# Kernel optimization log

Hardware: AMD Instinct MI355X
Metric: run time of the kernel (lower is better)

The kernel has to match this reference:

```python
import jax, jax.numpy as jnp
import numpy as np

EPS = 1e-6
ROPE_THETA = 10000.0


def rmsnorm(x, w):
    return x * jax.lax.rsqrt(jnp.mean(x * x, axis=-1, keepdims=True) + EPS) * w


def rope(q, k, seq_len, head_dim):
    # rotate-half RoPE. q,k: [b, h, s, d]
    half = head_dim // 2
    inv_freq = 1.0 / (ROPE_THETA ** (jnp.arange(0, half, dtype=jnp.float32) / half))
    t = jnp.arange(seq_len, dtype=jnp.float32)
    freqs = jnp.outer(t, inv_freq)                      # [s, d/2]
    cos = jnp.concatenate([jnp.cos(freqs)] * 2, axis=-1)  # [s, d]
    sin = jnp.concatenate([jnp.sin(freqs)] * 2, axis=-1)

    def rot(x):
        x1, x2 = x[..., :half], x[..., half:]
        return jnp.concatenate([-x2, x1], axis=-1)

    return q * cos + rot(q) * sin, k * cos + rot(k) * sin


def setup_inputs() -> dict:
    key = jax.random.key(0)
    ks = jax.random.split(key, 8)
    B, S, D, E, F = 4, 2048, 1024, 8, 4096
    sd = 0.02
    return {
        "x": jax.random.normal(ks[0], (B, S, D), dtype=jnp.float32),
        "mapped_tokens": jax.random.randint(ks[1], (B, S), 0, E, dtype=jnp.int32),
        "rms1_w": jnp.ones((D,), dtype=jnp.float32),
        "wqkv": jax.random.normal(ks[2], (D, 3 * D), dtype=jnp.float32) * sd,
        "wo": jax.random.normal(ks[3], (D, D), dtype=jnp.float32) * sd,
        "rms2_w": jnp.ones((D,), dtype=jnp.float32),
        "w1": jax.random.normal(ks[4], (E, D, F), dtype=jnp.float32) * sd,
        "w2": jax.random.normal(ks[5], (E, F, D), dtype=jnp.float32) * sd,
    }


def attention(x, wqkv, wo, num_heads=16):
    B, S, D = x.shape
    hd = D // num_heads
    qkv = x @ wqkv                                       # [b, s, 3D]
    q, k, v = jnp.split(qkv, 3, axis=-1)
    def heads(t):
        return t.reshape(B, S, num_heads, hd).transpose(0, 2, 1, 3)  # [b,h,s,d]
    q, k, v = heads(q), heads(k), heads(v)
    q, k = rope(q, k, S, hd)
    scores = jnp.einsum("bhqd,bhkd->bhqk", q, k) / jnp.sqrt(jnp.float32(hd))
    causal = jnp.tril(jnp.ones((S, S), dtype=bool))
    scores = jnp.where(causal, scores, jnp.finfo(scores.dtype).min)
    attn = jax.nn.softmax(scores, axis=-1)
    out = jnp.einsum("bhqk,bhkd->bhqd", attn, v)
    out = out.transpose(0, 2, 1, 3).reshape(B, S, D)
    return out @ wo


def moe_hash_ffn(x, mapped_tokens, w1, w2):
    # hash-routed MoE: each token goes to exactly one expert given by mapped_tokens
    B, S, D = x.shape
    E = w1.shape[0]
    xf = x.reshape(B * S, D)
    mt = mapped_tokens.reshape(B * S)
    out = jnp.zeros_like(xf)
    for e in range(E):  # small fixed expert count
        y = jax.nn.gelu(xf @ w1[e]) @ w2[e]
        out = out + jnp.where((mt == e)[:, None], y, 0.0)
    return out.reshape(B, S, D)


def reference(x, mapped_tokens, rms1_w, wqkv, wo, rms2_w, w1, w2):
    h = x + attention(rmsnorm(x, rms1_w), wqkv, wo)
    out = h + moe_hash_ffn(rmsnorm(h, rms2_w), mapped_tokens, w1, w2)
    return out
```

## Files before the change

kernel.cpp:

```cpp
#include <hip/hip_runtime.h>
#include <hip/hip_bf16.h>
#include <stdint.h>

typedef __hip_bfloat16 bf16;
typedef __attribute__((ext_vector_type(8))) short bf16x8;
typedef __attribute__((ext_vector_type(4))) float f32x4;
typedef __attribute__((ext_vector_type(16))) float f32x16;
typedef unsigned int u32;

static constexpr int Bsz = 4, S = 2048, D = 1024, E = 8, F = 4096, NH = 16, HD = 64;
static constexpr int TOK = Bsz * S;
static constexpr int SLOTS = TOK + E * 128;

#define DEV __device__ __forceinline__

DEV void async16(const bf16* g, bf16* l) {
  __builtin_amdgcn_global_load_lds((const __attribute__((address_space(1))) u32*)g,
                                   (__attribute__((address_space(3))) u32*)l, 16, 0, 0);
}

DEV u32 lds_off(const bf16* p) {
  return (u32)(uintptr_t)(__attribute__((address_space(3))) bf16*)p;
}

DEV bf16x8 dsr128(u32 addr) {
  bf16x8 d;
  asm volatile("ds_read_b128 %0, %1" : "=v"(d) : "v"(addr));
  return d;
}

DEV float gelu_fast(float x) {
  const float z = 0.7978845608028654f * (x + 0.044715f * x * x * x);
  return x / (1.f + __expf(-2.f * z));
}

DEV u32 cvtpk(float lo, float hi) {
  u32 r;
  asm("v_cvt_pk_bf16_f32 %0, %1, %2" : "=v"(r) : "v"(lo), "v"(hi));
  return r;
}


__global__ void cvt_transpose(const float* __restrict__ in, bf16* __restrict__ out, int R, int C) {
  __shared__ float t[64][65];
  const size_t zoff = (size_t)blockIdx.z * R * C;
  const int c0 = blockIdx.x * 64, r0 = blockIdx.y * 64;
  const int tid = threadIdx.x;
  const int lrow = tid >> 4, lcol = (tid & 15) * 4;
#pragma unroll
  for (int p = 0; p < 4; ++p) {
    const int r = lrow + p * 16;
    const float4 v = *(const float4*)(in + zoff + (size_t)(r0 + r) * C + c0 + lcol);
    t[r][lcol] = v.x; t[r][lcol + 1] = v.y; t[r][lcol + 2] = v.z; t[r][lcol + 3] = v.w;
  }
  __syncthreads();
  const int ow = tid >> 3, je = (tid & 7) * 8;
#pragma unroll
  for (int p = 0; p < 2; ++p) {
    const int oc = ow + p * 32;
    union { bf16x8 v; bf16 b[8]; } o8;
#pragma unroll
    for (int j = 0; j < 8; ++j) o8.b[j] = __float2bfloat16(t[je + j][oc]);
    *(bf16x8*)(out + zoff + (size_t)(c0 + oc) * R + r0 + je) = o8.v;
  }
}

__global__ void rope_tables(float* __restrict__ cosT, float* __restrict__ sinT) {
  const int s = blockIdx.x * 2 + (threadIdx.x >> 5);
  const int i = threadIdx.x & 31;
  const float inv_freq = powf(10000.f, -(float)i / 32.f);
  const float ang = (float)s * inv_freq;
  cosT[s * 32 + i] = cosf(ang);
  sinT[s * 32 + i] = sinf(ang);
}

__global__ void rmsnorm_k(const float* __restrict__ x, const float* __restrict__ w, bf16* __restrict__ out) {
  const size_t row = blockIdx.x;
  const int tid = threadIdx.x;
  const float4 v = *(const float4*)(x + row * D + tid * 4);
  float ss = v.x * v.x + v.y * v.y + v.z * v.z + v.w * v.w;
#pragma unroll
  for (int off = 1; off < 64; off <<= 1) ss += __shfl_xor(ss, off);
  __shared__ float red[4];
  if ((tid & 63) == 0) red[tid >> 6] = ss;
  __syncthreads();
  const float inv = rsqrtf((red[0] + red[1] + red[2] + red[3]) * (1.f / D) + 1e-6f);
  const float4 wv = *(const float4*)(w + tid * 4);
  union { ushort4 u; bf16 b[4]; } o;
  o.b[0] = __float2bfloat16(v.x * inv * wv.x);
  o.b[1] = __float2bfloat16(v.y * inv * wv.y);
  o.b[2] = __float2bfloat16(v.z * inv * wv.z);
  o.b[3] = __float2bfloat16(v.w * inv * wv.w);
  *(ushort4*)((unsigned short*)out + row * D + tid * 4) = o.u;
}

__global__ void route_init(int* counts, int* cursors, int* perm) {
  const int i = blockIdx.x * 256 + threadIdx.x;
  if (i < E) { counts[i] = 0; cursors[i] = 0; }
  if (i < SLOTS) perm[i] = -1;
}
__global__ void route_count(const int* __restrict__ mt, int* counts) {
  const int i = blockIdx.x * 256 + threadIdx.x;
  if (i < TOK) atomicAdd(&counts[mt[i]], 1);
}
__global__ void route_offsets(const int* __restrict__ counts, int* aoff) {
  if (threadIdx.x == 0) {
    int off = 0; aoff[0] = 0;
    for (int e = 0; e < E; ++e) { off += (counts[e] + 127) & ~127; aoff[e + 1] = off; }
  }
}
__global__ void route_scatter(const int* __restrict__ mt, const int* __restrict__ aoff,
                              int* cursors, int* perm) {
  const int i = blockIdx.x * 256 + threadIdx.x;
  if (i < TOK) { const int e = mt[i]; perm[aoff[e] + atomicAdd(&cursors[e], 1)] = i; }
}

__global__ __launch_bounds__(512) void qkv8p(
    const bf16* __restrict__ A, const bf16* __restrict__ Bt,
    const float* __restrict__ c_t, const float* __restrict__ s_t,
    bf16* __restrict__ o_q, bf16* __restrict__ o_k, bf16* __restrict__ o_v) {
  constexpr int K = 1024, NT = K / 64;
  __shared__ __align__(16) bf16 LA[2][256 * 64];
  __shared__ __align__(16) bf16 LB[2][256 * 64];
  const int tid = threadIdx.x;
  const int lane = tid & 63, wv = tid >> 6;
  const int wm = wv >> 2, wn = wv & 3;
  const int rl = lane & 15, kg = lane >> 4;
  const int gx = gridDim.x;
  const int nwg = gx * gridDim.y;
  int bid = blockIdx.y * gx + blockIdx.x;
  bid = (bid & 7) * (nwg >> 3) + (bid >> 3);
  const int nbase = (bid % gx) * 256, mbase = (bid / gx) * 256;
  f32x4 acc[8][4] = {};
  const int srow = tid >> 3;
  const int sc = (tid & 7) ^ ((srow >> 1) & 7);
  const bf16* Ag = A + (size_t)(mbase + srow) * K + sc * 8;
  const bf16* Bg = Bt + (size_t)(nbase + srow) * K + sc * 8;

  auto stage = [&](int t, int h) {
    const int buf = t & 1;
    const int mat = h >> 1, rh = h & 1;
    const bf16* src = (mat ? Bg : Ag) + (size_t)(rh * 128) * K + t * 64;
    bf16* dst = (mat ? &LB[buf][0] : &LA[buf][0]) + rh * 128 * 64 + tid * 8;
    async16(src, dst);
    async16(src + (size_t)64 * K, dst + 64 * 64);
  };

  bf16x8 bfr[4];
  auto phaseC = [&](int t, int ks, int mih, bool loadB) {
    const int buf = t & 1;
    const u32 ab = lds_off(&LA[buf][0]);
    const u32 bb = lds_off(&LB[buf][0]);
    bf16x8 af[4];
#pragma unroll
    for (int mi = 0; mi < 4; ++mi) {
      const int row = wm * 128 + mih * 64 + mi * 16 + rl;
      const u32 ph = (u32)((ks * 4 + kg) ^ ((row >> 1) & 7));
      af[mi] = dsr128(ab + (u32)row * 128 + ph * 16);
    }
    if (loadB) {
#pragma unroll
      for (int ni = 0; ni < 4; ++ni) {
        const int row = wn * 64 + ni * 16 + rl;
        const u32 ph = (u32)((ks * 4 + kg) ^ ((row >> 1) & 7));
        bfr[ni] = dsr128(bb + (u32)row * 128 + ph * 16);
      }
    }
    asm volatile("s_waitcnt lgkmcnt(0)" ::: "memory");
    __builtin_amdgcn_sched_barrier(0);
    __builtin_amdgcn_s_setprio(1);
#pragma unroll
    for (int mi = 0; mi < 4; ++mi)
#pragma unroll
      for (int ni = 0; ni < 4; ++ni)
        acc[mih * 4 + mi][ni] =
            __builtin_amdgcn_mfma_f32_16x16x32_bf16(af[mi], bfr[ni], acc[mih * 4 + mi][ni], 0, 0, 0);
    __builtin_amdgcn_s_setprio(0);
  };

  stage(0, 0); stage(0, 1); stage(0, 2); stage(0, 3);
  for (int t = 0; t < NT; ++t) {
    const bool more = (t + 1 < NT);
#pragma unroll
    for (int p = 0; p < 4; ++p) {
      if (p == 0) {
        if (more) {
          stage(t + 1, 0);
          asm volatile("s_waitcnt vmcnt(2)" ::: "memory");
        } else {
          asm volatile("s_waitcnt vmcnt(0)" ::: "memory");
        }
        __builtin_amdgcn_s_barrier();
        __builtin_amdgcn_sched_barrier(0);
      } else if (more) {
        stage(t + 1, p);
      }
      phaseC(t, p >> 1, p & 1, (p & 1) == 0);
      __builtin_amdgcn_s_barrier();
      __builtin_amdgcn_sched_barrier(0);
    }
  }

  const int colbase = nbase + wn * 64;
  const int part = colbase >> 10;
  const int head = (colbase & 1023) >> 6;
  const float qs = (part == 0) ? 0.18033688011112042f : 1.f;
#pragma unroll
  for (int ai = 0; ai < 8; ++ai) {
    const int rowoff = (ai >> 2) * 64 + (ai & 3) * 16;
#pragma unroll
    for (int r = 0; r < 4; ++r) {
      const int grow = mbase + wm * 128 + rowoff + kg * 4 + r;
      const int bb = grow >> 11, sp = grow & (S - 1);
      if (part == 2) {
#pragma unroll
        for (int ni = 0; ni < 4; ++ni) {
          const int d = ni * 16 + rl;
          o_v[((size_t)(bb * NH + head) * HD + d) * S + sp] = __float2bfloat16(acc[ai][ni][r]);
        }
      } else {
        bf16* dst = (part == 0) ? o_q : o_k;
        const size_t base = ((size_t)(bb * NH + head) * S + sp) * HD;
#pragma unroll
        for (int np = 0; np < 2; ++np) {
          const int i = np * 16 + rl;
          const float c = c_t[sp * 32 + i];
          const float sn = s_t[sp * 32 + i];
          const float lo = acc[ai][np][r];
          const float hi = acc[ai][np + 2][r];
          dst[base + i] = __float2bfloat16((lo * c - hi * sn) * qs);
          dst[base + i + 32] = __float2bfloat16((hi * c + lo * sn) * qs);
        }
      }
    }
  }
}

template <int EPI, int BM>
__global__ __launch_bounds__(2 * BM) void gemm_bt(
    const bf16* __restrict__ A, const bf16* __restrict__ Bt, int M, int N, int K,
    const int* __restrict__ aoff, long long estride,
    const float* __restrict__ xres, float* __restrict__ o_h,
    bf16* __restrict__ o_act,
    const int* __restrict__ perm, const float* __restrict__ hres, float* __restrict__ o_out) {
  constexpr int WN = BM / 64;
  constexpr int MR = BM / 2;
  constexpr int M_FR = MR / 16;
  __shared__ __align__(16) bf16 As[2][BM * 32];
  __shared__ __align__(16) bf16 Bs[2][BM * 32];
  const int tid = threadIdx.x;
  const int lane = tid & 63, wv = tid >> 6;
  const int wm = wv / WN, wn = wv % WN;
  const int rl = lane & 15, kg = lane >> 4;
  const int gx = gridDim.x;
  const int nwg = gx * gridDim.y;
  int bid = blockIdx.y * gx + blockIdx.x;
  bid = (bid & 7) * (nwg >> 3) + (bid >> 3);
  const int nbase = (bid % gx) * BM, mbase = (bid / gx) * BM;
  const bf16* Btp = Bt;
  if constexpr (EPI >= 2) {
    int e = 0;
#pragma unroll
    for (int t = 0; t < E - 1; ++t) e += (mbase >= aoff[t + 1]) ? 1 : 0;
    Btp = Bt + (size_t)e * estride;
  }
  f32x4 acc[M_FR][4] = {};
  const int srow = tid >> 2;
  const int sc = (tid & 3) ^ ((srow >> 1) & 3);
  const bf16* Agp[2];
#pragma unroll
  for (int c = 0; c < 2; ++c) {
    int rowslot = mbase + c * MR + srow;
    if constexpr (EPI == 2) {
      const int t = perm[rowslot];
      rowslot = (t < 0) ? 0 : t;
    }
    Agp[c] = A + (size_t)rowslot * K + sc * 8;
  }
  const bf16* Bg = Btp + (size_t)(nbase + srow) * K + sc * 8;

  auto stage = [&](int bi, int ko) {
#pragma unroll
    for (int c = 0; c < 2; ++c) {
      async16(Agp[c] + ko, &As[bi][c * MR * 32 + wv * 512]);
      async16(Bg + (size_t)(c * MR) * K + ko, &Bs[bi][c * MR * 32 + wv * 512]);
    }
  };
  auto compute = [&](int bi) {
    bf16x8 af[M_FR], bfr[4];
#pragma unroll
    for (int mi = 0; mi < M_FR; ++mi) {
      const int row = wm * MR + mi * 16 + rl;
      af[mi] = *(const bf16x8*)&As[bi][row * 32 + ((kg ^ ((row >> 1) & 3))) * 8];
    }
#pragma unroll
    for (int ni = 0; ni < 4; ++ni) {
      const int row = wn * 64 + ni * 16 + rl;
      bfr[ni] = *(const bf16x8*)&Bs[bi][row * 32 + ((kg ^ ((row >> 1) & 3))) * 8];
    }
#pragma unroll
    for (int mi = 0; mi < M_FR; ++mi)
#pragma unroll
      for (int ni = 0; ni < 4; ++ni)
        acc[mi][ni] = __builtin_amdgcn_mfma_f32_16x16x32_bf16(af[mi], bfr[ni], acc[mi][ni], 0, 0, 0);
  };

  const int nk = K >> 5;
  stage(0, 0);
  __syncthreads();
  for (int kb = 0; kb < nk; ++kb) {
    if (kb + 1 < nk) stage((kb + 1) & 1, (kb + 1) * 32);
    compute(kb & 1);
    __syncthreads();
  }

#pragma unroll
  for (int mi = 0; mi < M_FR; ++mi) {
#pragma unroll
    for (int ni = 0; ni < 4; ++ni) {
#pragma unroll
      for (int r = 0; r < 4; ++r) {
        const int grow = mbase + wm * MR + mi * 16 + kg * 4 + r;
        const int gcol = nbase + wn * 64 + ni * 16 + rl;
        const float vv = acc[mi][ni][r];
        if constexpr (EPI == 1) {
          const size_t ix = (size_t)grow * 1024 + gcol;
          o_h[ix] = xres[ix] + vv;
        } else if constexpr (EPI == 2) {
          o_act[(size_t)grow * 4096 + gcol] = __float2bfloat16(gelu_fast(vv));
        } else {
          const int t = perm[grow];
          if (t >= 0) {
            const size_t ix = (size_t)t * 1024 + gcol;
            o_out[ix] = hres[ix] + vv;
          }
        }
      }
    }
  }
}

__global__ __launch_bounds__(256, 3) void attn_kernel(const bf16* __restrict__ Qb,
                                                      const bf16* __restrict__ Kb,
                                                      const bf16* __restrict__ Vt,
                                                      bf16* __restrict__ AO) {
  __shared__ __align__(16) bf16 Kl[2][64 * 64];
  __shared__ __align__(16) bf16 Vl[2][64 * 64];
  const int bh = blockIdx.x;
  const int tid = threadIdx.x;
  const int w = tid >> 6, lane = tid & 63;
  const int q = lane & 31, hi = lane >> 5;
  const bf16* Qp = Qb + (size_t)bh * S * HD;
  const bf16* Kp = Kb + (size_t)bh * S * HD;
  const bf16* Vp = Vt + (size_t)bh * S * HD;
  const int b = bh >> 4, h = bh & 15;
  const int qblk = (S / 128 - 1) - blockIdx.y;
  const int qrow0 = qblk * 128 + w * 32;
  const int ntb = qblk * 2 + 2;
  const int ntw = (qrow0 >> 6) + 1;
  const int srow = tid >> 3;
  const int schk = tid & 7;

  bf16x8 qf[4];
#pragma unroll
  for (int t = 0; t < 4; ++t)
    qf[t] = *(const bf16x8*)(Qp + (size_t)(qrow0 + q) * HD + t * 16 + hi * 8);
  f32x16 oa0 = {}, oa1 = {};
  float m = -INFINITY, l = 0.f;

  auto stageKV = [&](int buf, int kvb) {
#pragma unroll
    for (int hh = 0; hh < 2; ++hh) {
      const int row = srow + hh * 32;
      const int c = schk ^ (row & 7);
      async16(Kp + (size_t)(kvb + row) * HD + c * 8, &Kl[buf][tid * 8 + hh * 2048]);
      async16(Vp + (size_t)row * S + kvb + c * 8, &Vl[buf][tid * 8 + hh * 2048]);
    }
  };
  auto packP = [&](float s0, float s1, float s2, float s3,
                   float s4, float s5, float s6, float s7) -> bf16x8 {
    u32 x0 = cvtpk(s0, s1), x1 = cvtpk(s2, s3);
    u32 y0 = cvtpk(s4, s5), y1 = cvtpk(s6, s7);
    asm volatile("v_permlane32_swap_b32 %0, %1" : "+v"(x0), "+v"(y0));
    asm volatile("v_permlane32_swap_b32 %0, %1" : "+v"(x1), "+v"(y1));
    union { u32 w[4]; bf16x8 v; } u;
    u.w[0] = x0; u.w[1] = x1; u.w[2] = y0; u.w[3] = y1;
    return u.v;
  };

  stageKV(0, 0);
  __syncthreads();
  for (int kt = 0; kt < ntb; ++kt) {
    const int buf = kt & 1;
    const int kvb = kt * 64;
    if (kt + 1 < ntb) stageKV(buf ^ 1, kvb + 64);
    if (kt < ntw) {
      f32x16 sa0 = {}, sa1 = {};
#pragma unroll
      for (int t = 0; t < 4; ++t) {
        const int c = (2 * t + hi) ^ (q & 7);
        const bf16x8 kf0 = *(const bf16x8*)&Kl[buf][q * 64 + c * 8];
        sa0 = __builtin_amdgcn_mfma_f32_32x32x16_bf16(kf0, qf[t], sa0, 0, 0, 0);
      }
#pragma unroll
      for (int t = 0; t < 4; ++t) {
        const int c = (2 * t + hi) ^ (q & 7);
        const bf16x8 kf1 = *(const bf16x8*)&Kl[buf][(q + 32) * 64 + c * 8];
        sa1 = __builtin_amdgcn_mfma_f32_32x32x16_bf16(kf1, qf[t], sa1, 0, 0, 0);
      }
      if (kvb + 63 > qrow0) {
#pragma unroll
        for (int r = 0; r < 16; ++r) {
          const int kloc = (r & 3) + 8 * (r >> 2) + 4 * hi;
          sa0[r] = (kvb + kloc > qrow0 + q) ? -3.0e38f : sa0[r];
          sa1[r] = (kvb + 32 + kloc > qrow0 + q) ? -3.0e38f : sa1[r];
        }
      }
      float vm;
      {
        float a0 = fmaxf(fmaxf(sa0[0], sa0[1]), fmaxf(sa0[2], sa0[3]));
        float a1 = fmaxf(fmaxf(sa0[4], sa0[5]), fmaxf(sa0[6], sa0[7]));
        float a2 = fmaxf(fmaxf(sa0[8], sa0[9]), fmaxf(sa0[10], sa0[11]));
        float a3 = fmaxf(fmaxf(sa0[12], sa0[13]), fmaxf(sa0[14], sa0[15]));
        float b0 = fmaxf(fmaxf(sa1[0], sa1[1]), fmaxf(sa1[2], sa1[3]));
        float b1 = fmaxf(fmaxf(sa1[4], sa1[5]), fmaxf(sa1[6], sa1[7]));
        float b2 = fmaxf(fmaxf(sa1[8], sa1[9]), fmaxf(sa1[10], sa1[11]));
        float b3 = fmaxf(fmaxf(sa1[12], sa1[13]), fmaxf(sa1[14], sa1[15]));
        vm = fmaxf(fmaxf(fmaxf(a0, a1), fmaxf(a2, a3)), fmaxf(fmaxf(b0, b1), fmaxf(b2, b3)));
      }
      vm = fmaxf(vm, __shfl_xor(vm, 32));
      const bool grow = __any(vm > m);
      const float mn = grow ? fmaxf(m, vm) : m;
#pragma unroll
      for (int r = 0; r < 16; ++r) {
        sa0[r] = exp2f(sa0[r] - mn);
        sa1[r] = exp2f(sa1[r] - mn);
      }
      float ps;
      {
        float a0 = (sa0[0] + sa0[1]) + (sa0[2] + sa0[3]);
        float a1 = (sa0[4] + sa0[5]) + (sa0[6] + sa0[7]);
        float a2 = (sa0[8] + sa0[9]) + (sa0[10] + sa0[11]);
        float a3 = (sa0[12] + sa0[13]) + (sa0[14] + sa0[15]);
        float b0 = (sa1[0] + sa1[1]) + (sa1[2] + sa1[3]);
        float b1 = (sa1[4] + sa1[5]) + (sa1[6] + sa1[7]);
        float b2 = (sa1[8] + sa1[9]) + (sa1[10] + sa1[11]);
        float b3 = (sa1[12] + sa1[13]) + (sa1[14] + sa1[15]);
        ps = ((a0 + a1) + (a2 + a3)) + ((b0 + b1) + (b2 + b3));
      }
      ps += __shfl_xor(ps, 32);
      if (grow) {
        const float scs = exp2f(m - mn);
        l = l * scs + ps;
        m = mn;
#pragma unroll
        for (int r = 0; r < 16; ++r) { oa0[r] *= scs; oa1[r] *= scs; }
      } else {
        l += ps;
      }
      {
        auto vrd = [&](int r, int s2i) -> bf16x8 {
          const int c = (2 * s2i + hi) ^ (r & 7);
          return *(const bf16x8*)&Vl[buf][r * 64 + c * 8];
        };
        const bf16x8 pf0 = packP(sa0[0], sa0[1], sa0[2], sa0[3], sa0[4], sa0[5], sa0[6], sa0[7]);
        oa0 = __builtin_amdgcn_mfma_f32_32x32x16_bf16(vrd(q, 0), pf0, oa0, 0, 0, 0);
        oa1 = __builtin_amdgcn_mfma_f32_32x32x16_bf16(vrd(q + 32, 0), pf0, oa1, 0, 0, 0);
        const bf16x8 pf1 = packP(sa0[8], sa0[9], sa0[10], sa0[11], sa0[12], sa0[13], sa0[14], sa0[15]);
        oa0 = __builtin_amdgcn_mfma_f32_32x32x16_bf16(vrd(q, 1), pf1, oa0, 0, 0, 0);
        oa1 = __builtin_amdgcn_mfma_f32_32x32x16_bf16(vrd(q + 32, 1), pf1, oa1, 0, 0, 0);
        const bf16x8 pf2 = packP(sa1[0], sa1[1], sa1[2], sa1[3], sa1[4], sa1[5], sa1[6], sa1[7]);
        oa0 = __builtin_amdgcn_mfma_f32_32x32x16_bf16(vrd(q, 2), pf2, oa0, 0, 0, 0);
        oa1 = __builtin_amdgcn_mfma_f32_32x32x16_bf16(vrd(q + 32, 2), pf2, oa1, 0, 0, 0);
        const bf16x8 pf3 = packP(sa1[8], sa1[9], sa1[10], sa1[11], sa1[12], sa1[13], sa1[14], sa1[15]);
        oa0 = __builtin_amdgcn_mfma_f32_32x32x16_bf16(vrd(q, 3), pf3, oa0, 0, 0, 0);
        oa1 = __builtin_amdgcn_mfma_f32_32x32x16_bf16(vrd(q + 32, 3), pf3, oa1, 0, 0, 0);
      }
    }
    __syncthreads();
  }
  const float invl = 1.f / l;
#pragma unroll
  for (int n = 0; n < 2; ++n) {
#pragma unroll
    for (int g = 0; g < 4; ++g) {
      union { ushort4 u4; bf16 bb[4]; } o4;
#pragma unroll
      for (int mi = 0; mi < 4; ++mi) {
        const float val = (n ? oa1[4 * g + mi] : oa0[4 * g + mi]) * invl;
        o4.bb[mi] = __float2bfloat16(val);
      }
      const int d = n * 32 + 8 * g + 4 * hi;
      *(ushort4*)&AO[((size_t)(b * S + qrow0 + q)) * D + h * HD + d] = o4.u4;
    }
  }
}

extern "C" void kernel_launch(void* const* d_in, const int* in_sizes, int n_in,
                              void* d_out, int out_size, void* d_ws, size_t ws_size,
                              hipStream_t stream) {
  const float* x = (const float*)d_in[0];
  const int* mt = (const int*)d_in[1];
  const float* rms1 = (const float*)d_in[2];
  const float* wqkv = (const float*)d_in[3];
  const float* wo = (const float*)d_in[4];
  const float* rms2 = (const float*)d_in[5];
  const float* w1 = (const float*)d_in[6];
  const float* w2 = (const float*)d_in[7];
  float* out = (float*)d_out;
  (void)in_sizes; (void)n_in; (void)out_size; (void)ws_size;

  char* ws = (char*)d_ws;
  size_t off = 0;
  auto alloc = [&](size_t b) { void* p = ws + off; off = (off + b + 255) & ~(size_t)255; return p; };
  bf16* wqkvT = (bf16*)alloc((size_t)3072 * 1024 * 2);
  bf16* woT   = (bf16*)alloc((size_t)1024 * 1024 * 2);
  bf16* w1T   = (bf16*)alloc((size_t)E * F * D * 2);
  bf16* w2T   = (bf16*)alloc((size_t)E * D * F * 2);
  float* cosT = (float*)alloc((size_t)S * 32 * 4);
  float* sinT = (float*)alloc((size_t)S * 32 * 4);
  float* hbuf = (float*)alloc((size_t)TOK * D * 4);
  bf16* xn2   = (bf16*)alloc((size_t)TOK * D * 2);
  int* counts  = (int*)alloc(E * 4);
  int* cursors = (int*)alloc(E * 4);
  int* aoff    = (int*)alloc((E + 1) * 4);
  int* perm    = (int*)alloc(SLOTS * 4);
  char* R = (char*)alloc((size_t)5 * TOK * D * 2);
  bf16* xn = (bf16*)R;
  bf16* qb = (bf16*)(R + (size_t)1 * TOK * D * 2);
  bf16* kb = (bf16*)(R + (size_t)2 * TOK * D * 2);
  bf16* vb = (bf16*)(R + (size_t)3 * TOK * D * 2);
  bf16* ao = (bf16*)(R + (size_t)4 * TOK * D * 2);
  bf16* act = (bf16*)R;

  cvt_transpose<<<dim3(3072 / 64, 1024 / 64, 1), 256, 0, stream>>>(wqkv, wqkvT, 1024, 3072);
  cvt_transpose<<<dim3(1024 / 64, 1024 / 64, 1), 256, 0, stream>>>(wo, woT, 1024, 1024);
  cvt_transpose<<<dim3(4096 / 64, 1024 / 64, E), 256, 0, stream>>>(w1, w1T, 1024, 4096);
  cvt_transpose<<<dim3(1024 / 64, 4096 / 64, E), 256, 0, stream>>>(w2, w2T, 4096, 1024);
  rope_tables<<<dim3(S / 2), 64, 0, stream>>>(cosT, sinT);
  route_init<<<dim3((SLOTS + 255) / 256), 256, 0, stream>>>(counts, cursors, perm);
  route_count<<<dim3(TOK / 256), 256, 0, stream>>>(mt, counts);
  route_offsets<<<dim3(1), 64, 0, stream>>>(counts, aoff);
  route_scatter<<<dim3(TOK / 256), 256, 0, stream>>>(mt, aoff, cursors, perm);
  rmsnorm_k<<<dim3(TOK), 256, 0, stream>>>(x, rms1, xn);
  qkv8p<<<dim3(3072 / 256, TOK / 256), 512, 0, stream>>>(
      xn, wqkvT, cosT, sinT, qb, kb, vb);
  attn_kernel<<<dim3(64, S / 128), 256, 0, stream>>>(qb, kb, vb, ao);
  gemm_bt<1, 128><<<dim3(1024 / 128, TOK / 128), 256, 0, stream>>>(
      ao, woT, TOK, 1024, 1024, nullptr, 0, x, hbuf, nullptr, nullptr, nullptr, nullptr);
  rmsnorm_k<<<dim3(TOK), 256, 0, stream>>>(hbuf, rms2, xn2);
  gemm_bt<2, 128><<<dim3(4096 / 128, SLOTS / 128), 256, 0, stream>>>(
      xn2, w1T, SLOTS, 4096, 1024, aoff, (long long)F * D, nullptr, nullptr, act, perm,
      nullptr, nullptr);
  gemm_bt<3, 128><<<dim3(1024 / 128, SLOTS / 128), 256, 0, stream>>>(
      act, w2T, SLOTS, 1024, 4096, aoff, (long long)D * F, nullptr, nullptr, nullptr, perm,
      hbuf, out);
}
```

Before: 625.6 us.

## Replace MoE expert GEMMs with 256x256 eight-phase pipelined kernel

Adds an ffn8p kernel for the two expert GEMMs, modeled on the qkv8p design: 256x256 tiles, 512 threads, 64-wide K steps, double-buffered async global-to-LDS loads interleaved with four compute phases, XOR swizzle, and setprio around MFMA. Expert padding is raised from 128 to 256 slots so each tile maps to a single expert. Blocks beyond the last used slot now exit early. The larger tiles cut global reloads of A and B per FLOP, at the cost of more padding work and fewer workgroups. gemm_bt is reduced to handle only the output-projection epilogue.

```diff
diff --git a/kernel.cpp b/kernel.cpp
--- a/kernel.cpp
+++ b/kernel.cpp
@@ -10,7 +10,7 @@
 
 static constexpr int Bsz = 4, S = 2048, D = 1024, E = 8, F = 4096, NH = 16, HD = 64;
 static constexpr int TOK = Bsz * S;
-static constexpr int SLOTS = TOK + E * 128;
+static constexpr int SLOTS = TOK + E * 256;
 
 #define DEV __device__ __forceinline__
 
@@ -106,7 +106,7 @@
 __global__ void route_offsets(const int* __restrict__ counts, int* aoff) {
   if (threadIdx.x == 0) {
     int off = 0; aoff[0] = 0;
-    for (int e = 0; e < E; ++e) { off += (counts[e] + 127) & ~127; aoff[e + 1] = off; }
+    for (int e = 0; e < E; ++e) { off += (counts[e] + 255) & ~255; aoff[e + 1] = off; }
   }
 }
 __global__ void route_scatter(const int* __restrict__ mt, const int* __restrict__ aoff,
@@ -236,13 +236,151 @@
   }
 }
 
+template <int EPI, int K>
+__global__ __launch_bounds__(512) void ffn8p(
+    const bf16* __restrict__ A, const bf16* __restrict__ Bt,
+    const int* __restrict__ aoff, long long estride,
+    bf16* __restrict__ o_act,
+    const int* __restrict__ perm, const float* __restrict__ hres,
+    float* __restrict__ o_out) {
+  constexpr int NT = K / 64;
+  __shared__ __align__(16) bf16 LA[2][256 * 64];
+  __shared__ __align__(16) bf16 LB[2][256 * 64];
+  const int tid = threadIdx.x;
+  const int lane = tid & 63, wv = tid >> 6;
+  const int wm = wv >> 2, wn = wv & 3;
+  const int rl = lane & 15, kg = lane >> 4;
+  const int gx = gridDim.x;
+  const int nwg = gx * gridDim.y;
+  int bid = blockIdx.y * gx + blockIdx.x;
+  bid = (bid & 7) * (nwg >> 3) + (bid >> 3);
+  const int nbase = (bid % gx) * 256, mbase = (bid / gx) * 256;
+  if (mbase >= aoff[E]) return;
+  int e = 0;
+#pragma unroll
+  for (int t = 0; t < E - 1; ++t) e += (mbase >= aoff[t + 1]) ? 1 : 0;
+  const bf16* Btp = Bt + (size_t)e * estride;
+
+  f32x4 acc[8][4] = {};
+  const int srow = tid >> 3;
+  const int sc = (tid & 7) ^ ((srow >> 1) & 7);
+  const bf16* Agr[4];
+#pragma unroll
+  for (int c = 0; c < 4; ++c) {
+    int slot = mbase + c * 64 + srow;
+    if constexpr (EPI == 2) { const int pt = perm[slot]; slot = (pt < 0) ? 0 : pt; }
+    Agr[c] = A + (size_t)slot * K + sc * 8;
+  }
+  const bf16* Bg = Btp + (size_t)(nbase + srow) * K + sc * 8;
+
+  auto stB = [&](int t, int hb) {
+    const int buf = t & 1;
+    bf16* dst = &LB[buf][0] + hb * 128 * 64 + tid * 8;
+    const bf16* src = Bg + (size_t)(hb * 128) * K + t * 64;
+    async16(src, dst);
+    async16(src + (size_t)64 * K, dst + 64 * 64);
+  };
+  auto stA = [&](int t, int ha) {
+    const int buf = t & 1;
+    bf16* dst = &LA[buf][0] + ha * 64 * 64 + tid * 8;
+    async16(Agr[ha] + t * 64, dst);
+    async16(Agr[ha + 2] + t * 64, dst + 128 * 64);
+  };
+
+  bf16x8 bfr[2][4];
+  auto phase = [&](int t, int q, bool loadB) {
+    const int buf = t & 1;
+    const u32 ab = lds_off(&LA[buf][0]);
+    const u32 bb = lds_off(&LB[buf][0]);
+    bf16x8 af[2][2];
+#pragma unroll
+    for (int j = 0; j < 2; ++j) {
+      const int row = wm * 128 + (2 * q + j) * 16 + rl;
+#pragma unroll
+      for (int ks = 0; ks < 2; ++ks) {
+        const u32 ch = (u32)((ks * 4 + kg) ^ ((row >> 1) & 7));
+        af[j][ks] = dsr128(ab + (u32)row * 128 + ch * 16);
+      }
+    }
+    if (loadB) {
+#pragma unroll
+      for (int ks = 0; ks < 2; ++ks)
+#pragma unroll
+        for (int ni = 0; ni < 4; ++ni) {
+          const int row = wn * 64 + ni * 16 + rl;
+          const u32 ch = (u32)((ks * 4 + kg) ^ ((row >> 1) & 7));
+          bfr[ks][ni] = dsr128(bb + (u32)row * 128 + ch * 16);
+        }
+    }
+    asm volatile("s_waitcnt lgkmcnt(0)" ::: "memory");
+    __builtin_amdgcn_sched_barrier(0);
+    __builtin_amdgcn_s_setprio(1);
+#pragma unroll
+    for (int ks = 0; ks < 2; ++ks)
+#pragma unroll
+      for (int j = 0; j < 2; ++j)
+#pragma unroll
+        for (int ni = 0; ni < 4; ++ni)
+          acc[2 * q + j][ni] = __builtin_amdgcn_mfma_f32_16x16x32_bf16(
+              af[j][ks], bfr[ks][ni], acc[2 * q + j][ni], 0, 0, 0);
+    __builtin_amdgcn_s_setprio(0);
+  };
+
+  stB(0, 0); stB(0, 1); stA(0, 0); stA(0, 1);
+  if (NT > 1) { stB(1, 0); stB(1, 1); stA(1, 0); }
+  for (int t = 0; t < NT; ++t) {
+    if (t + 1 < NT) {
+      stA(t + 1, 1);
+      asm volatile("s_waitcnt vmcnt(8)" ::: "memory");
+    } else {
+      asm volatile("s_waitcnt vmcnt(0)" ::: "memory");
+    }
+    __builtin_amdgcn_s_barrier();
+    __builtin_amdgcn_sched_barrier(0);
+    phase(t, 0, true);
+    __builtin_amdgcn_s_barrier();
+    __builtin_amdgcn_sched_barrier(0);
+    if (t + 2 < NT) stB(t + 2, 0);
+    phase(t, 1, false);
+    __builtin_amdgcn_s_barrier();
+    __builtin_amdgcn_sched_barrier(0);
+    if (t + 2 < NT) stB(t + 2, 1);
+    phase(t, 2, false);
+    __builtin_amdgcn_s_barrier();
+    __builtin_amdgcn_sched_barrier(0);
+    if (t + 2 < NT) stA(t + 2, 0);
+    phase(t, 3, false);
+    __builtin_amdgcn_s_barrier();
+    __builtin_amdgcn_sched_barrier(0);
+  }
+
+#pragma unroll
+  for (int mi = 0; mi < 8; ++mi) {
+#pragma unroll
+    for (int ni = 0; ni < 4; ++ni) {
+#pragma unroll
+      for (int r = 0; r < 4; ++r) {
+        const int grow = mbase + wm * 128 + mi * 16 + kg * 4 + r;
+        const int gcol = nbase + wn * 64 + ni * 16 + rl;
+        const float vv = acc[mi][ni][r];
+        if constexpr (EPI == 2) {
+          o_act[(size_t)grow * 4096 + gcol] = __float2bfloat16(gelu_fast(vv));
+        } else {
+          const int tk = perm[grow];
+          if (tk >= 0) {
+            const size_t ix = (size_t)tk * 1024 + gcol;
+            o_out[ix] = hres[ix] + vv;
+          }
+        }
+      }
+    }
+  }
+}
+
 template <int EPI, int BM>
 __global__ __launch_bounds__(2 * BM) void gemm_bt(
     const bf16* __restrict__ A, const bf16* __restrict__ Bt, int M, int N, int K,
-    const int* __restrict__ aoff, long long estride,
-    const float* __restrict__ xres, float* __restrict__ o_h,
-    bf16* __restrict__ o_act,
-    const int* __restrict__ perm, const float* __restrict__ hres, float* __restrict__ o_out) {
+    const float* __restrict__ xres, float* __restrict__ o_h) {
   constexpr int WN = BM / 64;
   constexpr int MR = BM / 2;
   constexpr int M_FR = MR / 16;
@@ -257,27 +395,13 @@
   int bid = blockIdx.y * gx + blockIdx.x;
   bid = (bid & 7) * (nwg >> 3) + (bid >> 3);
   const int nbase = (bid % gx) * BM, mbase = (bid / gx) * BM;
-  const bf16* Btp = Bt;
-  if constexpr (EPI >= 2) {
-    int e = 0;
-#pragma unroll
-    for (int t = 0; t < E - 1; ++t) e += (mbase >= aoff[t + 1]) ? 1 : 0;
-    Btp = Bt + (size_t)e * estride;
-  }
   f32x4 acc[M_FR][4] = {};
   const int srow = tid >> 2;
   const int sc = (tid & 3) ^ ((srow >> 1) & 3);
   const bf16* Agp[2];
 #pragma unroll
-  for (int c = 0; c < 2; ++c) {
-    int rowslot = mbase + c * MR + srow;
-    if constexpr (EPI == 2) {
-      const int t = perm[rowslot];
-      rowslot = (t < 0) ? 0 : t;
-    }
-    Agp[c] = A + (size_t)rowslot * K + sc * 8;
-  }
-  const bf16* Bg = Btp + (size_t)(nbase + srow) * K + sc * 8;
+  for (int c = 0; c < 2; ++c) Agp[c] = A + (size_t)(mbase + c * MR + srow) * K + sc * 8;
+  const bf16* Bg = Bt + (size_t)(nbase + srow) * K + sc * 8;
 
   auto stage = [&](int bi, int ko) {
 #pragma unroll
@@ -322,19 +446,8 @@
       for (int r = 0; r < 4; ++r) {
         const int grow = mbase + wm * MR + mi * 16 + kg * 4 + r;
         const int gcol = nbase + wn * 64 + ni * 16 + rl;
-        const float vv = acc[mi][ni][r];
-        if constexpr (EPI == 1) {
-          const size_t ix = (size_t)grow * 1024 + gcol;
-          o_h[ix] = xres[ix] + vv;
-        } else if constexpr (EPI == 2) {
-          o_act[(size_t)grow * 4096 + gcol] = __float2bfloat16(gelu_fast(vv));
-        } else {
-          const int t = perm[grow];
-          if (t >= 0) {
-            const size_t ix = (size_t)t * 1024 + gcol;
-            o_out[ix] = hres[ix] + vv;
-          }
-        }
+        const size_t ix = (size_t)grow * 1024 + gcol;
+        o_h[ix] = xres[ix] + acc[mi][ni][r];
       }
     }
   }
@@ -547,12 +660,10 @@
       xn, wqkvT, cosT, sinT, qb, kb, vb);
   attn_kernel<<<dim3(64, S / 128), 256, 0, stream>>>(qb, kb, vb, ao);
   gemm_bt<1, 128><<<dim3(1024 / 128, TOK / 128), 256, 0, stream>>>(
-      ao, woT, TOK, 1024, 1024, nullptr, 0, x, hbuf, nullptr, nullptr, nullptr, nullptr);
+      ao, woT, TOK, 1024, 1024, x, hbuf);
   rmsnorm_k<<<dim3(TOK), 256, 0, stream>>>(hbuf, rms2, xn2);
-  gemm_bt<2, 128><<<dim3(4096 / 128, SLOTS / 128), 256, 0, stream>>>(
-      xn2, w1T, SLOTS, 4096, 1024, aoff, (long long)F * D, nullptr, nullptr, act, perm,
-      nullptr, nullptr);
-  gemm_bt<3, 128><<<dim3(1024 / 128, SLOTS / 128), 256, 0, stream>>>(
-      act, w2T, SLOTS, 1024, 4096, aoff, (long long)D * F, nullptr, nullptr, nullptr, perm,
-      hbuf, out);
-}
+  ffn8p<2, 1024><<<dim3(4096 / 256, SLOTS / 256), 512, 0, stream>>>(
+      xn2, w1T, aoff, (long long)F * D, act, perm, nullptr, nullptr);
+  ffn8p<3, 4096><<<dim3(1024 / 256, SLOTS / 256), 512, 0, stream>>>(
+      act, w2T, aoff, (long long)D * F, nullptr, perm, hbuf, out);
+}
```

After: 674.1 us. +7.8%, slower.
